# Performance work log

Measured on AMD Instinct MI355X. Metric: run time of the kernel, lower is better.

Reference implementation:

```python
import jax, jax.numpy as jnp
import numpy as np

# Model hyperparameters (match init_kwargs)
NUM_HEADS = 12
KEY_SIZE = 64
VALUE_SIZE = 64
D_MODEL = 768
NUM_LAYERS = 4
FFW = 3072
B, T, L = 2, 32, 256
LN_EPS = 1e-5


def _layer_norm(x, scale, offset):
    m = jnp.mean(x, axis=-1, keepdims=True)
    v = jnp.mean(jnp.square(x - m), axis=-1, keepdims=True)
    return (x - m) * jax.lax.rsqrt(v + LN_EPS) * scale + offset


def _axial_attn(x, Wq, Wk, Wv, Wo, bo, mode):
    # x: [B, T, L, D]
    b, t, l, d = x.shape
    q = (x @ Wq).reshape(b, t, l, NUM_HEADS, KEY_SIZE)
    k = (x @ Wk).reshape(b, t, l, NUM_HEADS, KEY_SIZE)
    v = (x @ Wv).reshape(b, t, l, NUM_HEADS, VALUE_SIZE)
    inv_sqrt_d = KEY_SIZE ** (-0.5)
    if mode == 'time':
        logits = jnp.einsum('btlhd,bTlhd->blhtT', q, k) * inv_sqrt_d
        w = jax.nn.softmax(logits, axis=-1)
        a = jnp.einsum('blhtT,bTlhd->btlhd', w, v)
    else:  # space
        logits = jnp.einsum('btlhd,btLhd->bthlL', q, k) * inv_sqrt_d
        w = jax.nn.softmax(logits, axis=-1)
        a = jnp.einsum('bthlL,btLhd->btlhd', w, v)
    a = a.reshape(b, t, l, NUM_HEADS * VALUE_SIZE)
    return a @ Wo + bo


def _forward(input_embeddings, Wq_t, Wk_t, Wv_t, Wo_t, bo_t,
             Wq_s, Wk_s, Wv_s, Wo_s, bo_s,
             ln_t_scale, ln_t_bias, ln_s_scale, ln_s_bias,
             ln2_scale, ln2_bias, W1, b1, W2, b2):
    def block(h, p):
        (wq_t, wk_t, wv_t, wo_t, bot, wq_s, wk_s, wv_s, wo_s, bos,
         lts, ltb, lss, lsb, l2s, l2b, w1, bb1, w2, bb2) = p
        # time attention + residual
        x = _layer_norm(h, lts, ltb)
        h = h + _axial_attn(x, wq_t, wk_t, wv_t, wo_t, bot, 'time')
        # space attention + residual
        x = _layer_norm(h, lss, lsb)
        h = h + _axial_attn(x, wq_s, wk_s, wv_s, wo_s, bos, 'space')
        # FFN + residual
        x = _layer_norm(h, l2s, l2b)
        ff = jax.nn.gelu(x @ w1 + bb1) @ w2 + bb2
        return h + ff, None

    params = (Wq_t, Wk_t, Wv_t, Wo_t, bo_t, Wq_s, Wk_s, Wv_s, Wo_s, bo_s,
              ln_t_scale, ln_t_bias, ln_s_scale, ln_s_bias,
              ln2_scale, ln2_bias, W1, b1, W2, b2)
    h, _ = jax.lax.scan(block, input_embeddings, params)
    return h


def setup_inputs() -> dict:
    key = jax.random.key(0)
    ks = jax.random.split(key, 32)
    D, H, KD, VD, F, NL = D_MODEL, NUM_HEADS, KEY_SIZE, VALUE_SIZE, FFW, NUM_LAYERS
    init_scale = 2.0 / np.sqrt(NL)  # VarianceScaling scale used by the module
    s_in = np.sqrt(init_scale / D).astype(np.float32)   # fan_in = D
    s_out = np.sqrt(init_scale / (H * VD)).astype(np.float32)
    s_ffw2 = np.sqrt(init_scale / F).astype(np.float32)
    x = jax.random.normal(ks[0], (B, T, L, D), dtype=jnp.float32)
    def nrm(k, shape, s):
        return jax.random.normal(k, shape, dtype=jnp.float32) * s
    inp = {
        'input_embeddings': x,
        'Wq_t': nrm(ks[1], (NL, D, H * KD), s_in),
        'Wk_t': nrm(ks[2], (NL, D, H * KD), s_in),
        'Wv_t': nrm(ks[3], (NL, D, H * VD), s_in),
        'Wo_t': nrm(ks[4], (NL, H * VD, D), s_out),
        'bo_t': jnp.zeros((NL, D), jnp.float32),
        'Wq_s': nrm(ks[5], (NL, D, H * KD), s_in),
        'Wk_s': nrm(ks[6], (NL, D, H * KD), s_in),
        'Wv_s': nrm(ks[7], (NL, D, H * VD), s_in),
        'Wo_s': nrm(ks[8], (NL, H * VD, D), s_out),
        'bo_s': jnp.zeros((NL, D), jnp.float32),
        'ln_t_scale': jnp.ones((NL, D), jnp.float32),
        'ln_t_bias': jnp.zeros((NL, D), jnp.float32),
        'ln_s_scale': jnp.ones((NL, D), jnp.float32),
        'ln_s_bias': jnp.zeros((NL, D), jnp.float32),
        'ln2_scale': jnp.ones((NL, D), jnp.float32),
        'ln2_bias': jnp.zeros((NL, D), jnp.float32),
        'W1': nrm(ks[9], (NL, D, F), s_in),
        'b1': jnp.zeros((NL, F), jnp.float32),
        'W2': nrm(ks[10], (NL, F, D), s_ffw2),
        'b2': jnp.zeros((NL, D), jnp.float32),
    }
    return inp


def reference(input_embeddings, Wq_t, Wk_t, Wv_t, Wo_t, bo_t,
              Wq_s, Wk_s, Wv_s, Wo_s, bo_s,
              ln_t_scale, ln_t_bias, ln_s_scale, ln_s_bias,
              ln2_scale, ln2_bias, W1, b1, W2, b2):
    return _forward(input_embeddings, Wq_t, Wk_t, Wv_t, Wo_t, bo_t,
                    Wq_s, Wk_s, Wv_s, Wo_s, bo_s,
                    ln_t_scale, ln_t_bias, ln_s_scale, ln_s_bias,
                    ln2_scale, ln2_bias, W1, b1, W2, b2)
```

## Files before the change

### kernel.cpp

```cpp
#include <hip/hip_runtime.h>


#define AS1 __attribute__((address_space(1)))
#define AS3 __attribute__((address_space(3)))

using bf16x8 = __attribute__((ext_vector_type(8))) short;
using f32x4  = __attribute__((ext_vector_type(4))) float;

__device__ __forceinline__ f32x4 mfma_bf16(bf16x8 a, bf16x8 b, f32x4 c) {
  return __builtin_amdgcn_mfma_f32_16x16x32_bf16(a, b, c, 0, 0, 0);
}

__device__ __forceinline__ void async16(const void* g, void* l) {
  __builtin_amdgcn_global_load_lds((const AS1 void*)g, (AS3 void*)l, 16, 0, 0);
}

__device__ __forceinline__ short f2bs(float f) {
  union { float f; unsigned u; } x; x.f = f;
  unsigned r = x.u + 0x7fffu + ((x.u >> 16) & 1u);
  return (short)(r >> 16);
}

__device__ __forceinline__ f32x4 fzero() {
  f32x4 v; v[0] = 0.f; v[1] = 0.f; v[2] = 0.f; v[3] = 0.f; return v;
}

__device__ __forceinline__ float quad16_max(float v) {
  v = fmaxf(v, __shfl_xor(v, 1));
  v = fmaxf(v, __shfl_xor(v, 2));
  v = fmaxf(v, __shfl_xor(v, 4));
  v = fmaxf(v, __shfl_xor(v, 8));
  return v;
}
__device__ __forceinline__ float quad16_sum(float v) {
  v += __shfl_xor(v, 1); v += __shfl_xor(v, 2);
  v += __shfl_xor(v, 4); v += __shfl_xor(v, 8);
  return v;
}

template<int MODE>
__global__ __launch_bounds__(512, 2) void gemm256(
    const short* __restrict__ A, const short* __restrict__ BT,
    const float* __restrict__ bias, const float* __restrict__ resid,
    float* __restrict__ outF, short* __restrict__ outB,
    int M, int N, int K, int nx)
{
  __shared__ __align__(16) short lds[65536];
  (void)M;
  const int tid  = threadIdx.x;
  const int lane = tid & 63, wave = tid >> 6;
  const int quad = lane >> 4, l16 = lane & 15;
  const int wm = wave >> 2, wn = wave & 3;

  const unsigned flat = blockIdx.x;
  const unsigned su = flat >> 3;
  const unsigned nxu = (unsigned)nx;
  const long bm0 = (long)((flat & 7u) + 8u * (su / nxu)) * 256;
  const long bn0 = (long)(su % nxu) * 256;

  const int trow = tid >> 3;
  const int tg   = ((tid & 7) ^ (trow & 7)) * 8;
  const short* As = A  + (bm0 + trow) * (long)K + tg;
  const short* Bs = BT + (bn0 + trow) * (long)K + tg;

  auto STAGE = [&](int tile, int isB, int half) {
    const short* sp = (isB ? Bs : As) + (long)half * 128 * K + (long)tile * 64;
    char* db = (char*)lds + (tile & 1) * 65536 + isB * 32768 + half * 16384
             + (tid << 4);
    async16(sp, db);
    async16(sp + ((long)K << 6), db + 8192);
  };

  const int swg   = (quad ^ (l16 & 7)) * 8;
  const int arow0 = wm * 128 + l16;
  const int brow0 = wn * 64 + l16;

  f32x4 acc[8][4];
#pragma unroll
  for (int i = 0; i < 8; ++i)
#pragma unroll
    for (int j = 0; j < 4; ++j) acc[i][j] = fzero();

  const int nt = K >> 6;

  STAGE(0, 0, 0); STAGE(0, 0, 1); STAGE(0, 1, 0); STAGE(0, 1, 1);
  asm volatile("s_waitcnt vmcnt(0)" ::: "memory");
  __builtin_amdgcn_s_barrier();
  __builtin_amdgcn_sched_barrier(0);

  for (int u = 0; u < nt; ++u) {
    const short* bufA = lds + (u & 1) * 32768;
    const short* bufB = bufA + 16384;
    const bool pf = (u + 1 < nt);
    bf16x8 a[4][2], b[4][2];

    if (pf) STAGE(u + 1, 0, 0);
#pragma unroll
    for (int i = 0; i < 4; ++i) {
      a[i][0] = *(const bf16x8*)(bufA + (arow0 + i * 16) * 64 + swg);
      a[i][1] = *(const bf16x8*)(bufA + (arow0 + i * 16) * 64 + (swg ^ 32));
    }
#pragma unroll
    for (int j = 0; j < 2; ++j) {
      b[j][0] = *(const bf16x8*)(bufB + (brow0 + j * 16) * 64 + swg);
      b[j][1] = *(const bf16x8*)(bufB + (brow0 + j * 16) * 64 + (swg ^ 32));
    }
    asm volatile("s_waitcnt lgkmcnt(0)" ::: "memory");
    __builtin_amdgcn_sched_barrier(0);
    __builtin_amdgcn_s_setprio(1);
#pragma unroll
    for (int kk = 0; kk < 2; ++kk)
#pragma unroll
      for (int i = 0; i < 4; ++i)
#pragma unroll
        for (int j = 0; j < 2; ++j)
          acc[i][j] = mfma_bf16(a[i][kk], b[j][kk], acc[i][j]);
    __builtin_amdgcn_s_setprio(0);

    if (pf) STAGE(u + 1, 0, 1);
#pragma unroll
    for (int j = 2; j < 4; ++j) {
      b[j][0] = *(const bf16x8*)(bufB + (brow0 + j * 16) * 64 + swg);
      b[j][1] = *(const bf16x8*)(bufB + (brow0 + j * 16) * 64 + (swg ^ 32));
    }
    asm volatile("s_waitcnt lgkmcnt(0)" ::: "memory");
    __builtin_amdgcn_sched_barrier(0);
    __builtin_amdgcn_s_setprio(1);
#pragma unroll
    for (int kk = 0; kk < 2; ++kk)
#pragma unroll
      for (int i = 0; i < 4; ++i)
#pragma unroll
        for (int j = 2; j < 4; ++j)
          acc[i][j] = mfma_bf16(a[i][kk], b[j][kk], acc[i][j]);
    __builtin_amdgcn_s_setprio(0);

    if (pf) STAGE(u + 1, 1, 0);
#pragma unroll
    for (int i = 0; i < 4; ++i) {
      a[i][0] = *(const bf16x8*)(bufA + (arow0 + 64 + i * 16) * 64 + swg);
      a[i][1] = *(const bf16x8*)(bufA + (arow0 + 64 + i * 16) * 64 + (swg ^ 32));
    }
    asm volatile("s_waitcnt lgkmcnt(0)" ::: "memory");
    __builtin_amdgcn_sched_barrier(0);
    __builtin_amdgcn_s_setprio(1);
#pragma unroll
    for (int kk = 0; kk < 2; ++kk)
#pragma unroll
      for (int i = 0; i < 4; ++i)
#pragma unroll
        for (int j = 2; j < 4; ++j)
          acc[4 + i][j] = mfma_bf16(a[i][kk], b[j][kk], acc[4 + i][j]);
    __builtin_amdgcn_s_setprio(0);

    if (pf) STAGE(u + 1, 1, 1);
    __builtin_amdgcn_s_setprio(1);
#pragma unroll
    for (int kk = 0; kk < 2; ++kk)
#pragma unroll
      for (int i = 0; i < 4; ++i)
#pragma unroll
        for (int j = 0; j < 2; ++j)
          acc[4 + i][j] = mfma_bf16(a[i][kk], b[j][kk], acc[4 + i][j]);
    __builtin_amdgcn_s_setprio(0);
    asm volatile("s_waitcnt vmcnt(0)" ::: "memory");
    __builtin_amdgcn_s_barrier();
    __builtin_amdgcn_sched_barrier(0);
  }

  const long rowbase = bm0 + wm * 128 + quad * 4;
  const long colbase = bn0 + wn * 64 + l16;
#pragma unroll
  for (int i = 0; i < 8; ++i)
#pragma unroll
    for (int j = 0; j < 4; ++j) {
      const long gc = colbase + j * 16;
#pragma unroll
      for (int r = 0; r < 4; ++r) {
        const long gr = rowbase + i * 16 + r;
        const size_t idx = (size_t)gr * N + gc;
        float v = acc[i][j][r];
        if (MODE == 0) {
          outB[idx] = f2bs(v);
        } else if (MODE == 1) {
          outF[idx] = v + bias[gc] + resid[idx];
        } else {
          float tt = v + bias[gc];
          float z = 0.7978845608f * (tt + 0.044715f * tt * tt * tt);
          float g = __fdividef(tt, 1.f + __expf(-2.f * z));
          outB[idx] = f2bs(g);
        }
      }
    }
}

__global__ __launch_bounds__(256) void ln_kernel(
    const float* __restrict__ h, const float* __restrict__ sc,
    const float* __restrict__ bi, short* __restrict__ out)
{
  const int row = blockIdx.x, tid = threadIdx.x;
  const float* hr = h + (long)row * 768;
  float x0 = hr[tid], x1 = hr[tid + 256], x2 = hr[tid + 512];
  __shared__ float red[4];
  float s = x0 + x1 + x2;
#pragma unroll
  for (int m = 32; m >= 1; m >>= 1) s += __shfl_xor(s, m);
  if ((tid & 63) == 0) red[tid >> 6] = s;
  __syncthreads();
  float mean = (red[0] + red[1] + red[2] + red[3]) * (1.f / 768.f);
  float d0 = x0 - mean, d1 = x1 - mean, d2 = x2 - mean;
  float q = d0 * d0 + d1 * d1 + d2 * d2;
#pragma unroll
  for (int m = 32; m >= 1; m >>= 1) q += __shfl_xor(q, m);
  __syncthreads();
  if ((tid & 63) == 0) red[tid >> 6] = q;
  __syncthreads();
  float var = (red[0] + red[1] + red[2] + red[3]) * (1.f / 768.f);
  float inv = rsqrtf(var + 1e-5f);
  long o = (long)row * 768;
  out[o + tid]       = f2bs(d0 * inv * sc[tid]       + bi[tid]);
  out[o + tid + 256] = f2bs(d1 * inv * sc[tid + 256] + bi[tid + 256]);
  out[o + tid + 512] = f2bs(d2 * inv * sc[tid + 512] + bi[tid + 512]);
}

__global__ __launch_bounds__(256) void transpose_w(
    const float* __restrict__ in, short* __restrict__ out, int Kd, int Nd,
    long inStride, long outStride)
{
  __shared__ float t[32][33];
  const int z = blockIdx.z;
  in  += (long)z * inStride;
  out += (long)z * outStride;
  const int n0 = blockIdx.x * 32, k0 = blockIdx.y * 32;
  const int r = threadIdx.x >> 5, c = threadIdx.x & 31;
#pragma unroll
  for (int rr = 0; rr < 4; ++rr)
    t[r + rr * 8][c] = in[(long)(k0 + r + rr * 8) * Nd + n0 + c];
  __syncthreads();
#pragma unroll
  for (int rr = 0; rr < 4; ++rr)
    out[(long)(n0 + r + rr * 8) * Kd + k0 + c] = f2bs(t[c][r + rr * 8]);
}

__global__ __launch_bounds__(256) void attn_space(
    const short* __restrict__ qkv, short* __restrict__ ao)
{
  __shared__ __align__(16) short VT[64 * 256];
  __shared__ __align__(16) short P[4][16 * 256];
  const int qt = blockIdx.x, hh = blockIdx.y, bt = blockIdx.z;
  const long tok0 = (long)bt * 256;
  const int tid = threadIdx.x, wave = tid >> 6, lane = tid & 63;
  const int quad = lane >> 4, l16 = lane & 15;

#pragma unroll
  for (int it = 0; it < 8; ++it) {
    int chunk = it * 256 + tid;
    int vl = chunk >> 3, d8 = (chunk & 7) * 8;
    bf16x8 v = *(const bf16x8*)(qkv + (tok0 + vl) * 2304 + 1536 + hh * 64 + d8);
#pragma unroll
    for (int e = 0; e < 8; ++e) VT[(d8 + e) * 256 + vl] = v[e];
  }

  const int qr = qt * 64 + wave * 16;
  bf16x8 qf[2];
#pragma unroll
  for (int kk = 0; kk < 2; ++kk)
    qf[kk] = *(const bf16x8*)(qkv + (tok0 + qr + l16) * 2304 + hh * 64 + kk * 32 + quad * 8);

  f32x4 S[16];
#pragma unroll
  for (int j = 0; j < 16; ++j) S[j] = fzero();
#pragma unroll
  for (int j = 0; j < 16; ++j)
#pragma unroll
    for (int kk = 0; kk < 2; ++kk) {
      bf16x8 kf = *(const bf16x8*)(qkv + (tok0 + j * 16 + l16) * 2304 + 768 + hh * 64 + kk * 32 + quad * 8);
      S[j] = mfma_bf16(qf[kk], kf, S[j]);
    }

#pragma unroll
  for (int r = 0; r < 4; ++r) {
    float m = -1e30f;
#pragma unroll
    for (int j = 0; j < 16; ++j) m = fmaxf(m, S[j][r]);
    m = quad16_max(m);
    float sum = 0.f;
#pragma unroll
    for (int j = 0; j < 16; ++j) {
      float e = __expf((S[j][r] - m) * 0.125f);
      S[j][r] = e; sum += e;
    }
    sum = quad16_sum(sum);
    float inv = 1.f / sum;
#pragma unroll
    for (int j = 0; j < 16; ++j)
      P[wave][(quad * 4 + r) * 256 + j * 16 + l16] = f2bs(S[j][r] * inv);
  }
  __syncthreads();

  f32x4 O[4];
#pragma unroll
  for (int jn = 0; jn < 4; ++jn) O[jn] = fzero();
  for (int kk = 0; kk < 8; ++kk) {
    bf16x8 pf = *(const bf16x8*)&P[wave][l16 * 256 + kk * 32 + quad * 8];
#pragma unroll
    for (int jn = 0; jn < 4; ++jn) {
      bf16x8 vf = *(const bf16x8*)&VT[(jn * 16 + l16) * 256 + kk * 32 + quad * 8];
      O[jn] = mfma_bf16(pf, vf, O[jn]);
    }
  }
#pragma unroll
  for (int jn = 0; jn < 4; ++jn)
#pragma unroll
    for (int r = 0; r < 4; ++r) {
      int row = qr + quad * 4 + r;
      ao[(tok0 + row) * 768 + hh * 64 + jn * 16 + l16] = f2bs(O[jn][r]);
    }
}

__global__ __launch_bounds__(64) void attn_time(
    const short* __restrict__ qkv, short* __restrict__ ao)
{
  __shared__ __align__(16) short VT[64 * 32];
  __shared__ __align__(16) short P[32 * 32];
  const int ll = blockIdx.x, hh = blockIdx.y, b = blockIdx.z;
  const int lane = threadIdx.x;
  const int quad = lane >> 4, l16 = lane & 15;
#define TOK(t) (((long)(b * 32 + (t))) * 256 + ll)

#pragma unroll
  for (int it = 0; it < 4; ++it) {
    int chunk = it * 64 + lane;
    int t = chunk >> 3, d8 = (chunk & 7) * 8;
    bf16x8 v = *(const bf16x8*)(qkv + TOK(t) * 2304 + 1536 + hh * 64 + d8);
#pragma unroll
    for (int e = 0; e < 8; ++e) VT[(d8 + e) * 32 + t] = v[e];
  }

  bf16x8 qf[2][2];
#pragma unroll
  for (int mi = 0; mi < 2; ++mi)
#pragma unroll
    for (int kk = 0; kk < 2; ++kk)
      qf[mi][kk] = *(const bf16x8*)(qkv + TOK(mi * 16 + l16) * 2304 + hh * 64 + kk * 32 + quad * 8);

  f32x4 S[2][2];
#pragma unroll
  for (int mi = 0; mi < 2; ++mi) { S[mi][0] = fzero(); S[mi][1] = fzero(); }
#pragma unroll
  for (int nj = 0; nj < 2; ++nj)
#pragma unroll
    for (int kk = 0; kk < 2; ++kk) {
      bf16x8 kf = *(const bf16x8*)(qkv + TOK(nj * 16 + l16) * 2304 + 768 + hh * 64 + kk * 32 + quad * 8);
#pragma unroll
      for (int mi = 0; mi < 2; ++mi)
        S[mi][nj] = mfma_bf16(qf[mi][kk], kf, S[mi][nj]);
    }

#pragma unroll
  for (int mi = 0; mi < 2; ++mi)
#pragma unroll
    for (int r = 0; r < 4; ++r) {
      float m = fmaxf(S[mi][0][r], S[mi][1][r]);
      m = quad16_max(m);
      float e0 = __expf((S[mi][0][r] - m) * 0.125f);
      float e1 = __expf((S[mi][1][r] - m) * 0.125f);
      float sum = quad16_sum(e0 + e1);
      float inv = 1.f / sum;
      P[(mi * 16 + quad * 4 + r) * 32 + l16]      = f2bs(e0 * inv);
      P[(mi * 16 + quad * 4 + r) * 32 + 16 + l16] = f2bs(e1 * inv);
    }
  __syncthreads();

  f32x4 O[2][4];
#pragma unroll
  for (int mi = 0; mi < 2; ++mi)
#pragma unroll
    for (int jn = 0; jn < 4; ++jn) O[mi][jn] = fzero();
#pragma unroll
  for (int mi = 0; mi < 2; ++mi) {
    bf16x8 pf = *(const bf16x8*)&P[(mi * 16 + l16) * 32 + quad * 8];
#pragma unroll
    for (int jn = 0; jn < 4; ++jn) {
      bf16x8 vf = *(const bf16x8*)&VT[(jn * 16 + l16) * 32 + quad * 8];
      O[mi][jn] = mfma_bf16(pf, vf, O[mi][jn]);
    }
  }
#pragma unroll
  for (int mi = 0; mi < 2; ++mi)
#pragma unroll
    for (int jn = 0; jn < 4; ++jn)
#pragma unroll
      for (int r = 0; r < 4; ++r) {
        int t = mi * 16 + quad * 4 + r;
        ao[TOK(t) * 768 + hh * 64 + jn * 16 + l16] = f2bs(O[mi][jn][r]);
      }
#undef TOK
}

extern "C" void kernel_launch(void* const* d_in, const int* in_sizes, int n_in,
                              void* d_out, int out_size, void* d_ws, size_t ws_size,
                              hipStream_t stream)
{
  const float* emb     = (const float*)d_in[0];
  const float* Wq_t    = (const float*)d_in[1];
  const float* Wk_t    = (const float*)d_in[2];
  const float* Wv_t    = (const float*)d_in[3];
  const float* Wo_t    = (const float*)d_in[4];
  const float* bo_t    = (const float*)d_in[5];
  const float* Wq_s    = (const float*)d_in[6];
  const float* Wk_s    = (const float*)d_in[7];
  const float* Wv_s    = (const float*)d_in[8];
  const float* Wo_s    = (const float*)d_in[9];
  const float* bo_s    = (const float*)d_in[10];
  const float* ln_t_sc = (const float*)d_in[11];
  const float* ln_t_bi = (const float*)d_in[12];
  const float* ln_s_sc = (const float*)d_in[13];
  const float* ln_s_bi = (const float*)d_in[14];
  const float* ln2_sc  = (const float*)d_in[15];
  const float* ln2_bi  = (const float*)d_in[16];
  const float* W1      = (const float*)d_in[17];
  const float* b1      = (const float*)d_in[18];
  const float* W2      = (const float*)d_in[19];
  const float* b2      = (const float*)d_in[20];

  const long M = 16384, D = 768, QN = 2304, F = 3072;
  char* ws = (char*)d_ws;
  size_t off = 0;
  auto alloc = [&](size_t b) { char* p = ws + off; off += (b + 255) & ~(size_t)255; return p; };
  short* qkvT_t = (short*)alloc((size_t)4 * QN * D * 2);
  short* qkvT_s = (short*)alloc((size_t)4 * QN * D * 2);
  short* woT_t  = (short*)alloc((size_t)4 * D * D * 2);
  short* woT_s  = (short*)alloc((size_t)4 * D * D * 2);
  short* w1T    = (short*)alloc((size_t)4 * F * D * 2);
  short* w2T    = (short*)alloc((size_t)4 * D * F * 2);
  short* xb     = (short*)alloc((size_t)M * D * 2);
  short* aob    = (short*)alloc((size_t)M * D * 2);
  short* big    = (short*)alloc((size_t)M * F * 2);
  float* h = (float*)d_out;

  hipMemcpyAsync(h, emb, (size_t)M * D * 4, hipMemcpyDeviceToDevice, stream);

  transpose_w<<<dim3(24, 24, 4), 256, 0, stream>>>(Wq_t, qkvT_t,             768, 768,  D * D, QN * D);
  transpose_w<<<dim3(24, 24, 4), 256, 0, stream>>>(Wk_t, qkvT_t + D * D,     768, 768,  D * D, QN * D);
  transpose_w<<<dim3(24, 24, 4), 256, 0, stream>>>(Wv_t, qkvT_t + 2 * D * D, 768, 768,  D * D, QN * D);
  transpose_w<<<dim3(24, 24, 4), 256, 0, stream>>>(Wq_s, qkvT_s,             768, 768,  D * D, QN * D);
  transpose_w<<<dim3(24, 24, 4), 256, 0, stream>>>(Wk_s, qkvT_s + D * D,     768, 768,  D * D, QN * D);
  transpose_w<<<dim3(24, 24, 4), 256, 0, stream>>>(Wv_s, qkvT_s + 2 * D * D, 768, 768,  D * D, QN * D);
  transpose_w<<<dim3(24, 24, 4), 256, 0, stream>>>(Wo_t, woT_t,              768, 768,  D * D, D * D);
  transpose_w<<<dim3(24, 24, 4), 256, 0, stream>>>(Wo_s, woT_s,              768, 768,  D * D, D * D);
  transpose_w<<<dim3(96, 24, 4), 256, 0, stream>>>(W1,   w1T,                768, 3072, D * F, F * D);
  transpose_w<<<dim3(24, 96, 4), 256, 0, stream>>>(W2,   w2T,                3072, 768, F * D, D * F);

  for (int l = 0; l < 4; ++l) {
    ln_kernel<<<16384, 256, 0, stream>>>(h, ln_t_sc + l * 768, ln_t_bi + l * 768, xb);
    gemm256<0><<<9 * 64, 512, 0, stream>>>(xb, qkvT_t + (long)l * QN * D,
        nullptr, nullptr, nullptr, big, 16384, 2304, 768, 9);
    attn_time<<<dim3(256, 12, 2), 64, 0, stream>>>(big, aob);
    gemm256<1><<<3 * 64, 512, 0, stream>>>(aob, woT_t + (long)l * D * D,
        bo_t + l * 768, h, h, nullptr, 16384, 768, 768, 3);
    ln_kernel<<<16384, 256, 0, stream>>>(h, ln_s_sc + l * 768, ln_s_bi + l * 768, xb);
    gemm256<0><<<9 * 64, 512, 0, stream>>>(xb, qkvT_s + (long)l * QN * D,
        nullptr, nullptr, nullptr, big, 16384, 2304, 768, 9);
    attn_space<<<dim3(4, 12, 64), 256, 0, stream>>>(big, aob);
    gemm256<1><<<3 * 64, 512, 0, stream>>>(aob, woT_s + (long)l * D * D,
        bo_s + l * 768, h, h, nullptr, 16384, 768, 768, 3);
    ln_kernel<<<16384, 256, 0, stream>>>(h, ln2_sc + l * 768, ln2_bi + l * 768, xb);
    gemm256<2><<<12 * 64, 512, 0, stream>>>(xb, w1T + (long)l * F * D,
        b1 + l * 3072, nullptr, nullptr, big, 16384, 3072, 768, 12);
    gemm256<1><<<3 * 64, 512, 0, stream>>>(big, w2T + (long)l * D * F,
        b2 + l * 768, h, h, nullptr, 16384, 768, 3072, 3);
  }
}
```

Before: 2.545 ms.

## Software-pipeline LDS fragment reads across GEMM k-iterations with partial lgkmcnt waits

The GEMM main loop now keeps separate register fragments for the two A halves and two B halves. It loads the next tile's first A/B fragments from LDS right after the barrier, before the last MFMA quadrant of the current tile runs. Full lgkmcnt(0) waits are replaced with partial waits, and the global-to-LDS prefetches are grouped into two bursts. The goal is to hide LDS read latency and the barrier behind MFMA work, at the cost of more live registers under the 512-thread, 2-block launch bound.

Measured after the change: 2.601 ms. 1.02x slower.

```diff
diff --git a/kernel.cpp b/kernel.cpp
--- a/kernel.cpp
+++ b/kernel.cpp
@@ -37,6 +37,10 @@
   v += __shfl_xor(v, 4); v += __shfl_xor(v, 8);
   return v;
 }
+
+#define LGKM(n) asm volatile("s_waitcnt lgkmcnt(" #n ")" ::: "memory"); \
+                __builtin_amdgcn_sched_barrier(0)
+#define SCHED_FENCE() __builtin_amdgcn_sched_barrier(0)
 
 template<int MODE>
 __global__ __launch_bounds__(512, 2) void gemm256(
@@ -83,90 +87,74 @@
 
   const int nt = K >> 6;
 
+  bf16x8 a0[4][2], a1[4][2], b0[2][2], b1[2][2];
+
+#define RD_A0(base)                                                           \
+  _Pragma("unroll") for (int i = 0; i < 4; ++i) {                             \
+    a0[i][0] = *(const bf16x8*)((base) + (arow0 + i * 16) * 64 + swg);        \
+    a0[i][1] = *(const bf16x8*)((base) + (arow0 + i * 16) * 64 + (swg ^ 32)); \
+  }
+#define RD_A1(base)                                                           \
+  _Pragma("unroll") for (int i = 0; i < 4; ++i) {                             \
+    a1[i][0] = *(const bf16x8*)((base) + (arow0 + 64 + i * 16) * 64 + swg);   \
+    a1[i][1] = *(const bf16x8*)((base) + (arow0 + 64 + i * 16) * 64 + (swg ^ 32)); \
+  }
+#define RD_B0(base)                                                           \
+  _Pragma("unroll") for (int j = 0; j < 2; ++j) {                             \
+    b0[j][0] = *(const bf16x8*)((base) + 16384 + (brow0 + j * 16) * 64 + swg);\
+    b0[j][1] = *(const bf16x8*)((base) + 16384 + (brow0 + j * 16) * 64 + (swg ^ 32)); \
+  }
+#define RD_B1(base)                                                           \
+  _Pragma("unroll") for (int j = 0; j < 2; ++j) {                             \
+    b1[j][0] = *(const bf16x8*)((base) + 16384 + (brow0 + 32 + j * 16) * 64 + swg); \
+    b1[j][1] = *(const bf16x8*)((base) + 16384 + (brow0 + 32 + j * 16) * 64 + (swg ^ 32)); \
+  }
+#define QUAD(AF, BF, IO, JO)                                                  \
+  __builtin_amdgcn_s_setprio(1);                                              \
+  _Pragma("unroll") for (int kk = 0; kk < 2; ++kk)                            \
+    _Pragma("unroll") for (int i = 0; i < 4; ++i)                             \
+      _Pragma("unroll") for (int j = 0; j < 2; ++j)                           \
+        acc[(IO) + i][(JO) + j] = mfma_bf16(AF[i][kk], BF[j][kk], acc[(IO) + i][(JO) + j]); \
+  __builtin_amdgcn_s_setprio(0)
+
   STAGE(0, 0, 0); STAGE(0, 0, 1); STAGE(0, 1, 0); STAGE(0, 1, 1);
   asm volatile("s_waitcnt vmcnt(0)" ::: "memory");
   __builtin_amdgcn_s_barrier();
-  __builtin_amdgcn_sched_barrier(0);
+  SCHED_FENCE();
+  RD_A0(lds); RD_B0(lds);
+  SCHED_FENCE();
 
   for (int u = 0; u < nt; ++u) {
-    const short* bufA = lds + (u & 1) * 32768;
-    const short* bufB = bufA + 16384;
+    const short* buf  = lds + (u & 1) * 32768;
+    const short* nbuf = lds + ((u + 1) & 1) * 32768;
     const bool pf = (u + 1 < nt);
-    bf16x8 a[4][2], b[4][2];
-
-    if (pf) STAGE(u + 1, 0, 0);
-#pragma unroll
-    for (int i = 0; i < 4; ++i) {
-      a[i][0] = *(const bf16x8*)(bufA + (arow0 + i * 16) * 64 + swg);
-      a[i][1] = *(const bf16x8*)(bufA + (arow0 + i * 16) * 64 + (swg ^ 32));
-    }
-#pragma unroll
-    for (int j = 0; j < 2; ++j) {
-      b[j][0] = *(const bf16x8*)(bufB + (brow0 + j * 16) * 64 + swg);
-      b[j][1] = *(const bf16x8*)(bufB + (brow0 + j * 16) * 64 + (swg ^ 32));
-    }
-    asm volatile("s_waitcnt lgkmcnt(0)" ::: "memory");
-    __builtin_amdgcn_sched_barrier(0);
-    __builtin_amdgcn_s_setprio(1);
-#pragma unroll
-    for (int kk = 0; kk < 2; ++kk)
-#pragma unroll
-      for (int i = 0; i < 4; ++i)
-#pragma unroll
-        for (int j = 0; j < 2; ++j)
-          acc[i][j] = mfma_bf16(a[i][kk], b[j][kk], acc[i][j]);
-    __builtin_amdgcn_s_setprio(0);
-
-    if (pf) STAGE(u + 1, 0, 1);
-#pragma unroll
-    for (int j = 2; j < 4; ++j) {
-      b[j][0] = *(const bf16x8*)(bufB + (brow0 + j * 16) * 64 + swg);
-      b[j][1] = *(const bf16x8*)(bufB + (brow0 + j * 16) * 64 + (swg ^ 32));
-    }
-    asm volatile("s_waitcnt lgkmcnt(0)" ::: "memory");
-    __builtin_amdgcn_sched_barrier(0);
-    __builtin_amdgcn_s_setprio(1);
-#pragma unroll
-    for (int kk = 0; kk < 2; ++kk)
-#pragma unroll
-      for (int i = 0; i < 4; ++i)
-#pragma unroll
-        for (int j = 2; j < 4; ++j)
-          acc[i][j] = mfma_bf16(a[i][kk], b[j][kk], acc[i][j]);
-    __builtin_amdgcn_s_setprio(0);
-
-    if (pf) STAGE(u + 1, 1, 0);
-#pragma unroll
-    for (int i = 0; i < 4; ++i) {
-      a[i][0] = *(const bf16x8*)(bufA + (arow0 + 64 + i * 16) * 64 + swg);
-      a[i][1] = *(const bf16x8*)(bufA + (arow0 + 64 + i * 16) * 64 + (swg ^ 32));
-    }
-    asm volatile("s_waitcnt lgkmcnt(0)" ::: "memory");
-    __builtin_amdgcn_sched_barrier(0);
-    __builtin_amdgcn_s_setprio(1);
-#pragma unroll
-    for (int kk = 0; kk < 2; ++kk)
-#pragma unroll
-      for (int i = 0; i < 4; ++i)
-#pragma unroll
-        for (int j = 2; j < 4; ++j)
-          acc[4 + i][j] = mfma_bf16(a[i][kk], b[j][kk], acc[4 + i][j]);
-    __builtin_amdgcn_s_setprio(0);
-
-    if (pf) STAGE(u + 1, 1, 1);
-    __builtin_amdgcn_s_setprio(1);
-#pragma unroll
-    for (int kk = 0; kk < 2; ++kk)
-#pragma unroll
-      for (int i = 0; i < 4; ++i)
-#pragma unroll
-        for (int j = 0; j < 2; ++j)
-          acc[4 + i][j] = mfma_bf16(a[i][kk], b[j][kk], acc[4 + i][j]);
-    __builtin_amdgcn_s_setprio(0);
-    asm volatile("s_waitcnt vmcnt(0)" ::: "memory");
-    __builtin_amdgcn_s_barrier();
-    __builtin_amdgcn_sched_barrier(0);
-  }
+
+    RD_B1(buf);
+    LGKM(4);
+    QUAD(a0, b0, 0, 0);
+    if (pf) { STAGE(u + 1, 0, 0); STAGE(u + 1, 0, 1); }
+    RD_A1(buf);
+    SCHED_FENCE();
+    LGKM(8);
+    QUAD(a0, b1, 0, 2);
+    if (pf) { STAGE(u + 1, 1, 0); STAGE(u + 1, 1, 1); }
+    LGKM(0);
+    QUAD(a1, b0, 4, 0);
+    if (pf) {
+      asm volatile("s_waitcnt vmcnt(0)" ::: "memory");
+      __builtin_amdgcn_s_barrier();
+      SCHED_FENCE();
+      RD_A0(nbuf); RD_B0(nbuf);
+      SCHED_FENCE();
+    }
+    QUAD(a1, b1, 4, 2);
+  }
+
+#undef RD_A0
+#undef RD_A1
+#undef RD_B0
+#undef RD_B1
+#undef QUAD
 
   const long rowbase = bm0 + wm * 128 + quad * 4;
   const long colbase = bn0 + wn * 64 + l16;
```
